# Kernel optimization log

Hardware: AMD Instinct MI355X
Metric: run time of the kernel (lower is better)

The kernel has to match this reference:

```python
import math
import jax, jax.numpy as jnp
import numpy as np

H = 16  # head_count

def setup_inputs() -> dict:
    key = jax.random.key(0)
    ks = jax.random.split(key, 7)
    B, S, D = 2, 2048, 1024
    query = jax.random.normal(ks[0], (B, S, D), dtype=jnp.float32)
    # mask: True = masked position (matches masked_fill_ semantics)
    mask = jax.random.randint(ks[1], (B, S, S), 0, 2) > 0
    scale = 1.0 / math.sqrt(D)  # xavier-ish init scale
    Wq = jax.random.normal(ks[2], (D, D), dtype=jnp.float32) * scale
    Wk = jax.random.normal(ks[3], (D, D), dtype=jnp.float32) * scale
    Wv = jax.random.normal(ks[4], (D, D), dtype=jnp.float32) * scale
    Wo = jax.random.normal(ks[5], (D, D), dtype=jnp.float32) * scale
    bo = jnp.zeros((D,), dtype=jnp.float32)
    return {"query": query, "mask": mask, "Wq": Wq, "Wk": Wk, "Wv": Wv, "Wo": Wo, "bo": bo}


def reference(query, mask, Wq, Wk, Wv, Wo, bo):
    B, S, D = query.shape
    dh = D // H

    def split_heads(x):  # [B,S,D] -> [B,H,S,dh]
        return x.reshape(B, S, H, dh).transpose(0, 2, 1, 3)

    # torch nn.Linear computes x @ W.T (bias-free for q/k/v)
    q = split_heads(query @ Wq.T) * (1.0 / math.sqrt(dh))
    k = split_heads(query @ Wk.T)
    v = split_heads(query @ Wv.T)

    scores = jnp.einsum('bhqd,bhkd->bhqk', q, k)           # [B,H,S,S]
    scores = jnp.where(mask[:, None, :, :], jnp.float32(-1e18), scores)
    weights = jax.nn.softmax(scores, axis=-1)               # dropout=0 -> identity
    ctx = jnp.einsum('bhqk,bhkd->bhqd', weights, v)         # [B,H,S,dh]
    ctx = ctx.transpose(0, 2, 1, 3).reshape(B, S, D)        # combine heads
    return ctx @ Wo.T + bo
```

## Files before the change

kernel.cpp:

```cpp
#include <hip/hip_runtime.h>

#define S_LEN 2048
#define D_MODEL 1024
#define NH 16
#define DH 64

typedef __bf16 bf16x8 __attribute__((ext_vector_type(8)));
typedef __bf16 bf16x4 __attribute__((ext_vector_type(4)));
typedef float f32x4 __attribute__((ext_vector_type(4)));

__device__ __forceinline__ unsigned short f2bf(float f) {
  unsigned int x = __float_as_uint(f);
  x += 0x7fffu + ((x >> 16) & 1u);
  return (unsigned short)(x >> 16);
}

__device__ __forceinline__ bf16x4 cvt4(f32x4 v) {
  return __builtin_convertvector(v, bf16x4);
}

__device__ __forceinline__ float exp2raw(float x) {
#if __has_builtin(__builtin_amdgcn_exp2f)
  return __builtin_amdgcn_exp2f(x);
#else
  return exp2f(x);
#endif
}

__device__ __forceinline__ f32x4 mfma16(bf16x8 a, bf16x8 b, f32x4 c) {
  return __builtin_amdgcn_mfma_f32_16x16x32_bf16(a, b, c, 0, 0, 0);
}

__device__ __forceinline__ void gl2lds(const unsigned short* g, unsigned short* l) {
  __builtin_amdgcn_global_load_lds(
      (__attribute__((address_space(1))) void*)g,
      (__attribute__((address_space(3))) void*)l, 16, 0, 0);
}

__global__ __launch_bounds__(256) void prep_kernel(
    const float* __restrict__ q, const float* __restrict__ wq,
    const float* __restrict__ wk, const float* __restrict__ wv,
    const float* __restrict__ wo, const int* __restrict__ mask,
    unsigned short* __restrict__ qbf, unsigned short* __restrict__ wbf,
    unsigned long long* __restrict__ bits) {
  const int bx = blockIdx.x;
  if (bx < 32768) {
    int i = bx * 256 + threadIdx.x;
    unsigned long long bal = __ballot(mask[i] != 0);
    if ((threadIdx.x & 63) == 0) bits[i >> 6] = bal;
  } else {
    const long t = (long)(bx - 32768) * 256 + threadIdx.x;
    const float* src;
    unsigned short* dst;
    long e;
    if (t < 524288) { src = q; dst = qbf; e = t * 8; }
    else {
      long u = t - 524288;
      int wi = (int)(u >> 17);
      e = (u & 131071) * 8;
      src = wi == 0 ? wq : wi == 1 ? wk : wi == 2 ? wv : wo;
      dst = wbf + (long)wi * 1048576;
    }
    float4 a = *(const float4*)(src + e);
    float4 b = *(const float4*)(src + e + 4);
    ushort4 p0 = {f2bf(a.x), f2bf(a.y), f2bf(a.z), f2bf(a.w)};
    ushort4 p1 = {f2bf(b.x), f2bf(b.y), f2bf(b.z), f2bf(b.w)};
    *(ushort4*)(dst + e) = p0;
    *(ushort4*)(dst + e + 4) = p1;
  }
}

__global__ __launch_bounds__(256) void gemm_qkv(
    const unsigned short* __restrict__ A, const unsigned short* __restrict__ W3,
    unsigned short* __restrict__ qb, unsigned short* __restrict__ kb,
    unsigned short* __restrict__ vt, float qscale) {
  __shared__ unsigned short As[128 * 64];
  __shared__ unsigned short Bs[128 * 64];
  const int tid = threadIdx.x, lane = tid & 63, wid = tid >> 6;
  const int wm = wid >> 1, wn = wid & 1;
  const int quad = lane >> 4, c = lane & 15, cx = c & 7;
  const int nG = blockIdx.x * 128;
  const int wi = nG >> 10, nn0 = nG & 1023;
  const int m0 = blockIdx.y * 128;
  const unsigned short* Bsrc = W3 + (size_t)wi * 1048576;
  const int srow = lane >> 3;
  const int schk = ((lane & 7) ^ srow) * 8;
  const unsigned short* ag = A + (size_t)(m0 + wid * 32 + srow) * 1024 + schk;
  const unsigned short* bg = Bsrc + (size_t)(nn0 + wid * 32 + srow) * 1024 + schk;
  f32x4 acc[4][4] = {};
  if (wi < 2) {
    for (int kk = 0; kk < 1024; kk += 64) {
#pragma unroll
      for (int i = 0; i < 4; ++i) {
        gl2lds(ag + (size_t)(i * 8) * 1024 + kk, &As[(wid * 32 + i * 8) * 64]);
        gl2lds(bg + (size_t)(i * 8) * 1024 + kk, &Bs[(wid * 32 + i * 8) * 64]);
      }
      __syncthreads();
#pragma unroll
      for (int kc = 0; kc < 2; ++kc) {
        bf16x8 a[4], b[4];
#pragma unroll
        for (int mt = 0; mt < 4; ++mt)
          a[mt] = *(const bf16x8*)(
              &As[(wm * 64 + mt * 16 + c) * 64 + ((kc * 4 + quad) ^ cx) * 8]);
#pragma unroll
        for (int nt = 0; nt < 4; ++nt)
          b[nt] = *(const bf16x8*)(
              &Bs[(wn * 64 + nt * 16 + c) * 64 + ((kc * 4 + quad) ^ cx) * 8]);
#pragma unroll
        for (int mt = 0; mt < 4; ++mt)
#pragma unroll
          for (int nt = 0; nt < 4; ++nt)
            acc[mt][nt] = mfma16(b[nt], a[mt], acc[mt][nt]);
      }
      __syncthreads();
    }
    unsigned short* dst = (wi == 0) ? qb : kb;
    const float sc = (wi == 0) ? qscale : 1.0f;
#pragma unroll
    for (int mt = 0; mt < 4; ++mt) {
#pragma unroll
      for (int nt = 0; nt < 4; ++nt) {
        const int ss = m0 + wm * 64 + mt * 16 + c;
        const int nS = nn0 + wn * 64 + nt * 16 + quad * 4;
        const int hh = nS >> 6, d0 = nS & 63;
        const int bb = ss >> 11, sl = ss & 2047;
        f32x4 v = acc[mt][nt] * sc;
        *(bf16x4*)(dst + (size_t)((bb * NH + hh) * S_LEN + sl) * DH + d0) =
            cvt4(v);
      }
    }
  } else {
    for (int kk = 0; kk < 1024; kk += 64) {
#pragma unroll
      for (int i = 0; i < 4; ++i) {
        gl2lds(ag + (size_t)(i * 8) * 1024 + kk, &As[(wid * 32 + i * 8) * 64]);
        gl2lds(bg + (size_t)(i * 8) * 1024 + kk, &Bs[(wid * 32 + i * 8) * 64]);
      }
      __syncthreads();
#pragma unroll
      for (int kc = 0; kc < 2; ++kc) {
        bf16x8 a[4], b[4];
#pragma unroll
        for (int mt = 0; mt < 4; ++mt)
          a[mt] = *(const bf16x8*)(
              &As[(wm * 64 + mt * 16 + c) * 64 + ((kc * 4 + quad) ^ cx) * 8]);
#pragma unroll
        for (int nt = 0; nt < 4; ++nt)
          b[nt] = *(const bf16x8*)(
              &Bs[(wn * 64 + nt * 16 + c) * 64 + ((kc * 4 + quad) ^ cx) * 8]);
#pragma unroll
        for (int mt = 0; mt < 4; ++mt)
#pragma unroll
          for (int nt = 0; nt < 4; ++nt)
            acc[mt][nt] = mfma16(a[mt], b[nt], acc[mt][nt]);
      }
      __syncthreads();
    }
#pragma unroll
    for (int mt = 0; mt < 4; ++mt) {
#pragma unroll
      for (int nt = 0; nt < 4; ++nt) {
        const int mb = m0 + wm * 64 + mt * 16 + quad * 4;
        const int n = nn0 + wn * 64 + nt * 16 + c;
        const int hh = n >> 6, d = n & 63;
        const int bb = mb >> 11, ss = mb & 2047;
        *(bf16x4*)(vt + (size_t)((bb * NH + hh) * DH + d) * S_LEN + ss) =
            cvt4(acc[mt][nt]);
      }
    }
  }
}

__global__ __launch_bounds__(256) void gemm_out(
    const unsigned short* __restrict__ A, const unsigned short* __restrict__ W,
    float* __restrict__ out, const float* __restrict__ bias) {
  __shared__ unsigned short As[128 * 64];
  __shared__ unsigned short Bs[64 * 64];
  const int tid = threadIdx.x, lane = tid & 63, wid = tid >> 6;
  const int wm = wid >> 1, wn = wid & 1;
  const int quad = lane >> 4, c = lane & 15, cx = c & 7;
  const int n0 = blockIdx.x * 64, m0 = blockIdx.y * 128;
  const int srow = lane >> 3;
  const int schk = ((lane & 7) ^ srow) * 8;
  const unsigned short* ag = A + (size_t)(m0 + wid * 32 + srow) * 1024 + schk;
  const unsigned short* bg = W + (size_t)(n0 + wid * 16 + srow) * 1024 + schk;
  f32x4 acc[4][2] = {};
  for (int kk = 0; kk < 1024; kk += 64) {
#pragma unroll
    for (int i = 0; i < 4; ++i)
      gl2lds(ag + (size_t)(i * 8) * 1024 + kk, &As[(wid * 32 + i * 8) * 64]);
#pragma unroll
    for (int i = 0; i < 2; ++i)
      gl2lds(bg + (size_t)(i * 8) * 1024 + kk, &Bs[(wid * 16 + i * 8) * 64]);
    __syncthreads();
#pragma unroll
    for (int kc = 0; kc < 2; ++kc) {
      bf16x8 a[4], b[2];
#pragma unroll
      for (int mt = 0; mt < 4; ++mt)
        a[mt] = *(const bf16x8*)(
            &As[(wm * 64 + mt * 16 + c) * 64 + ((kc * 4 + quad) ^ cx) * 8]);
#pragma unroll
      for (int nt = 0; nt < 2; ++nt)
        b[nt] = *(const bf16x8*)(
            &Bs[(wn * 32 + nt * 16 + c) * 64 + ((kc * 4 + quad) ^ cx) * 8]);
#pragma unroll
      for (int mt = 0; mt < 4; ++mt)
#pragma unroll
        for (int nt = 0; nt < 2; ++nt)
          acc[mt][nt] = mfma16(b[nt], a[mt], acc[mt][nt]);
    }
    __syncthreads();
  }
#pragma unroll
  for (int mt = 0; mt < 4; ++mt) {
#pragma unroll
    for (int nt = 0; nt < 2; ++nt) {
      const int m = m0 + wm * 64 + mt * 16 + c;
      const int n = n0 + wn * 32 + nt * 16 + quad * 4;
      f32x4 bv = *(const f32x4*)(bias + n);
      f32x4 r = acc[mt][nt] + bv;
      *(f32x4*)(out + (size_t)m * D_MODEL + n) = r;
    }
  }
}

__global__ __launch_bounds__(256, 2) void attn_kernel(
    const unsigned short* __restrict__ qb, const unsigned short* __restrict__ kb,
    const unsigned short* __restrict__ vt,
    const unsigned long long* __restrict__ mbits,
    unsigned short* __restrict__ ctx) {
  const int h = blockIdx.x, qt = blockIdx.y, b = blockIdx.z;
  const int bh = b * NH + h;
  const int tid = threadIdx.x, lane = tid & 63, wid = tid >> 6;
  const int quad = lane >> 4, c = lane & 15, cx = c & 7;
  const int qw = wid & 1, kh = wid >> 1;
  const int q0 = qt * 128;
  __shared__ __align__(16) unsigned short KVw[4][8192];
  __shared__ __align__(16) unsigned short Pbuf[4][16 * 72];

  const int qbase = q0 + qw * 64;
  const unsigned short* qp = qb + (size_t)(bh * S_LEN + qbase + c) * DH;
  bf16x8 bq[4][2];
#pragma unroll
  for (int sub = 0; sub < 4; ++sub) {
    bq[sub][0] = *(const bf16x8*)(qp + sub * 16 * DH + quad * 8);
    bq[sub][1] = *(const bf16x8*)(qp + sub * 16 * DH + 32 + quad * 8);
  }

  f32x4 o[4][4] = {};
  float lacc[4] = {0.f, 0.f, 0.f, 0.f};
  const unsigned long long* mq0 =
      mbits + (size_t)(b * S_LEN + qbase + c) * 32 + kh * 16;

  const int srow = lane >> 3;
  const int schk = ((lane & 7) ^ srow) * 8;
  unsigned short* Kw = KVw[wid];
  unsigned short* Vw = KVw[wid] + 4096;
  unsigned short* Pw = Pbuf[wid];

  const unsigned short* gK =
      kb + (size_t)(bh * S_LEN + kh * 1024 + srow) * DH + schk;
  const unsigned short* gV =
      vt + (size_t)(bh * DH + srow) * S_LEN + kh * 1024 + schk;

#pragma unroll
  for (int i = 0; i < 8; ++i) gl2lds(gK + (size_t)(i * 8) * DH, &Kw[i * 512]);
#pragma unroll
  for (int i = 0; i < 8; ++i)
    gl2lds(gV + (size_t)(i * 8) * S_LEN, &Vw[i * 512]);

  for (int kt = 0; kt < 1024; kt += 64) {
    asm volatile("s_waitcnt vmcnt(8)" ::: "memory");

    bf16x8 kf[8];
#pragma unroll
    for (int g = 0; g < 4; ++g) {
      const int rho = g * 16 + c;
      kf[2 * g] = *(const bf16x8*)(&Kw[rho * 64 + (quad ^ cx) * 8]);
      kf[2 * g + 1] = *(const bf16x8*)(&Kw[rho * 64 + ((4 + quad) ^ cx) * 8]);
    }

    const int mi = kt >> 6;
    bf16x8 bp[4][2];
#pragma unroll
    for (int sub = 0; sub < 4; ++sub) {
      f32x4 s[4];
#pragma unroll
      for (int g = 0; g < 4; ++g) {
        f32x4 z = {};
        z = mfma16(kf[2 * g], bq[sub][0], z);
        z = mfma16(kf[2 * g + 1], bq[sub][1], z);
        s[g] = z;
      }
      const unsigned long long w64 = mq0[sub * 512 + mi];
      const unsigned int wlo = (unsigned int)w64;
      const unsigned int whi = (unsigned int)(w64 >> 32);
      float lp = 0.f;
#pragma unroll
      for (int g = 0; g < 4; ++g) {
        const unsigned int bits =
            ((g & 2) ? whi : wlo) >> ((g & 1) * 16 + quad * 4);
        f32x4 p;
#pragma unroll
        for (int r = 0; r < 4; ++r) {
          const float e = exp2raw(s[g][r]);
          p[r] = ((bits >> r) & 1u) ? 0.f : e;
          lp += p[r];
        }
        *(bf16x4*)(&Pw[c * 72 + g * 16 + quad * 4]) = cvt4(p);
      }
      lacc[sub] += lp;
      bp[sub][0] = *(const bf16x8*)(&Pw[c * 72 + quad * 8]);
      bp[sub][1] = *(const bf16x8*)(&Pw[c * 72 + 32 + quad * 8]);
    }

    if (kt + 64 < 1024) {
#pragma unroll
      for (int i = 0; i < 8; ++i)
        gl2lds(gK + (size_t)(kt + 64 + i * 8) * DH, &Kw[i * 512]);
      asm volatile("s_waitcnt vmcnt(8)" ::: "memory");
    } else {
      asm volatile("s_waitcnt vmcnt(0)" ::: "memory");
    }

#pragma unroll
    for (int ks = 0; ks < 2; ++ks) {
#pragma unroll
      for (int nt = 0; nt < 4; ++nt) {
        bf16x8 av = *(const bf16x8*)(
            &Vw[(nt * 16 + c) * 64 + ((ks * 4 + quad) ^ cx) * 8]);
#pragma unroll
        for (int sub = 0; sub < 4; ++sub)
          o[sub][nt] = mfma16(av, bp[sub][ks], o[sub][nt]);
      }
    }
    asm volatile("s_waitcnt lgkmcnt(0)" ::: "memory");
    if (kt + 64 < 1024) {
#pragma unroll
      for (int i = 0; i < 8; ++i)
        gl2lds(gV + (size_t)(i * 8) * S_LEN + kt + 64, &Vw[i * 512]);
    }
  }

#pragma unroll
  for (int sub = 0; sub < 4; ++sub) {
    lacc[sub] += __shfl_xor(lacc[sub], 16, 64);
    lacc[sub] += __shfl_xor(lacc[sub], 32, 64);
  }

  __syncthreads();
  float* mrg = (float*)&KVw[0][0];
  float* ml = mrg + 8 * 1088;
  if (kh == 1) {
#pragma unroll
    for (int sub = 0; sub < 4; ++sub) {
      float* mo = mrg + (qw * 4 + sub) * 1088;
#pragma unroll
      for (int nt = 0; nt < 4; ++nt)
        *(f32x4*)(mo + c * 68 + nt * 16 + quad * 4) = o[sub][nt];
      if (quad == 0) ml[(qw * 4 + sub) * 16 + c] = lacc[sub];
    }
  }
  __syncthreads();
  if (kh == 0) {
#pragma unroll
    for (int sub = 0; sub < 4; ++sub) {
      const int pp = qw * 4 + sub;
      const float inv = 1.0f / (lacc[sub] + ml[pp * 16 + c]);
      const int q = qbase + sub * 16 + c;
      const float* mo = mrg + pp * 1088;
#pragma unroll
      for (int nt = 0; nt < 4; ++nt) {
        f32x4 ob = *(const f32x4*)(mo + c * 68 + nt * 16 + quad * 4);
        f32x4 rr = (o[sub][nt] + ob) * inv;
        *(bf16x4*)(ctx + (size_t)(b * S_LEN + q) * D_MODEL + h * DH + nt * 16 +
                   quad * 4) = cvt4(rr);
      }
    }
  }
}

extern "C" void kernel_launch(void* const* d_in, const int* in_sizes, int n_in,
                              void* d_out, int out_size, void* d_ws, size_t ws_size,
                              hipStream_t stream) {
  const float* query = (const float*)d_in[0];
  const int* mask = (const int*)d_in[1];
  const float* Wq = (const float*)d_in[2];
  const float* Wk = (const float*)d_in[3];
  const float* Wv = (const float*)d_in[4];
  const float* Wo = (const float*)d_in[5];
  const float* bo = (const float*)d_in[6];
  float* out = (float*)d_out;

  char* ws = (char*)d_ws;
  const size_t MB = 1024 * 1024;
  unsigned short* qbf = (unsigned short*)(ws);
  unsigned short* wbf = (unsigned short*)(ws + 8 * MB);
  unsigned short* qb = (unsigned short*)(ws + 16 * MB);
  unsigned short* kb = (unsigned short*)(ws + 24 * MB);
  unsigned short* vt = (unsigned short*)(ws + 32 * MB);
  unsigned long long* mb = (unsigned long long*)(ws + 40 * MB);
  unsigned short* ctx = qbf;

  prep_kernel<<<32768 + 4096, 256, 0, stream>>>(query, Wq, Wk, Wv, Wo, mask,
                                                qbf, wbf, mb);

  gemm_qkv<<<dim3(3072 / 128, 4096 / 128), 256, 0, stream>>>(
      qbf, wbf, qb, kb, vt, 0.18033688f);

  attn_kernel<<<dim3(NH, S_LEN / 128, 2), 256, 0, stream>>>(qb, kb, vt, mb,
                                                            ctx);

  gemm_out<<<dim3(1024 / 64, 4096 / 128), 256, 0, stream>>>(
      ctx, wbf + 3 * 1048576, out, bo);
}
```

Before: 224.6 us.

## Double-buffer GEMM K-tiles and prefetch attention mask words and K tiles earlier

The QKV and output GEMMs move from single-buffered 64-wide K tiles with two barriers per step to double-buffered 32-wide tiles with one barrier per step. The next tile's global-to-LDS copy is issued before the current tile is computed. The XOR swizzle is dropped, which may add LDS bank conflicts. In attention, the mask words for the next key tile are loaded one iteration ahead and the next K tile copy is issued before the softmax work, to hide load latency. This adds register pressure and relies on the hand-written vmcnt waits still counting the right loads.

```diff
diff --git a/kernel.cpp b/kernel.cpp
--- a/kernel.cpp
+++ b/kernel.cpp
@@ -74,46 +74,45 @@
     const unsigned short* __restrict__ A, const unsigned short* __restrict__ W3,
     unsigned short* __restrict__ qb, unsigned short* __restrict__ kb,
     unsigned short* __restrict__ vt, float qscale) {
-  __shared__ unsigned short As[128 * 64];
-  __shared__ unsigned short Bs[128 * 64];
+  __shared__ unsigned short As[2][128 * 32];
+  __shared__ unsigned short Bs[2][128 * 32];
   const int tid = threadIdx.x, lane = tid & 63, wid = tid >> 6;
   const int wm = wid >> 1, wn = wid & 1;
-  const int quad = lane >> 4, c = lane & 15, cx = c & 7;
+  const int quad = lane >> 4, c = lane & 15;
   const int nG = blockIdx.x * 128;
   const int wi = nG >> 10, nn0 = nG & 1023;
   const int m0 = blockIdx.y * 128;
-  const unsigned short* Bsrc = W3 + (size_t)wi * 1048576;
-  const int srow = lane >> 3;
-  const int schk = ((lane & 7) ^ srow) * 8;
-  const unsigned short* ag = A + (size_t)(m0 + wid * 32 + srow) * 1024 + schk;
-  const unsigned short* bg = Bsrc + (size_t)(nn0 + wid * 32 + srow) * 1024 + schk;
+  const int srow = lane >> 2, sc4 = (lane & 3) * 8;
+  const unsigned short* ag = A + (size_t)(m0 + wid * 32 + srow) * 1024 + sc4;
+  const unsigned short* bg =
+      W3 + (size_t)wi * 1048576 + (size_t)(nn0 + wid * 32 + srow) * 1024 + sc4;
   f32x4 acc[4][4] = {};
+  gl2lds(ag, &As[0][(wid * 32) * 32]);
+  gl2lds(ag + 16 * 1024, &As[0][(wid * 32 + 16) * 32]);
+  gl2lds(bg, &Bs[0][(wid * 32) * 32]);
+  gl2lds(bg + 16 * 1024, &Bs[0][(wid * 32 + 16) * 32]);
   if (wi < 2) {
-    for (int kk = 0; kk < 1024; kk += 64) {
-#pragma unroll
-      for (int i = 0; i < 4; ++i) {
-        gl2lds(ag + (size_t)(i * 8) * 1024 + kk, &As[(wid * 32 + i * 8) * 64]);
-        gl2lds(bg + (size_t)(i * 8) * 1024 + kk, &Bs[(wid * 32 + i * 8) * 64]);
-      }
+    for (int kk = 0; kk < 1024; kk += 32) {
+      const int pb = (kk >> 5) & 1;
       __syncthreads();
-#pragma unroll
-      for (int kc = 0; kc < 2; ++kc) {
-        bf16x8 a[4], b[4];
-#pragma unroll
-        for (int mt = 0; mt < 4; ++mt)
-          a[mt] = *(const bf16x8*)(
-              &As[(wm * 64 + mt * 16 + c) * 64 + ((kc * 4 + quad) ^ cx) * 8]);
+      if (kk + 32 < 1024) {
+        gl2lds(ag + kk + 32, &As[pb ^ 1][(wid * 32) * 32]);
+        gl2lds(ag + 16 * 1024 + kk + 32, &As[pb ^ 1][(wid * 32 + 16) * 32]);
+        gl2lds(bg + kk + 32, &Bs[pb ^ 1][(wid * 32) * 32]);
+        gl2lds(bg + 16 * 1024 + kk + 32, &Bs[pb ^ 1][(wid * 32 + 16) * 32]);
+      }
+      bf16x8 a[4], b[4];
+#pragma unroll
+      for (int mt = 0; mt < 4; ++mt)
+        a[mt] = *(const bf16x8*)(&As[pb][(wm * 64 + mt * 16 + c) * 32 + quad * 8]);
+#pragma unroll
+      for (int nt = 0; nt < 4; ++nt)
+        b[nt] = *(const bf16x8*)(&Bs[pb][(wn * 64 + nt * 16 + c) * 32 + quad * 8]);
+#pragma unroll
+      for (int mt = 0; mt < 4; ++mt)
 #pragma unroll
         for (int nt = 0; nt < 4; ++nt)
-          b[nt] = *(const bf16x8*)(
-              &Bs[(wn * 64 + nt * 16 + c) * 64 + ((kc * 4 + quad) ^ cx) * 8]);
-#pragma unroll
-        for (int mt = 0; mt < 4; ++mt)
-#pragma unroll
-          for (int nt = 0; nt < 4; ++nt)
-            acc[mt][nt] = mfma16(b[nt], a[mt], acc[mt][nt]);
-      }
-      __syncthreads();
+          acc[mt][nt] = mfma16(b[nt], a[mt], acc[mt][nt]);
     }
     unsigned short* dst = (wi == 0) ? qb : kb;
     const float sc = (wi == 0) ? qscale : 1.0f;
@@ -131,31 +130,27 @@
       }
     }
   } else {
-    for (int kk = 0; kk < 1024; kk += 64) {
-#pragma unroll
-      for (int i = 0; i < 4; ++i) {
-        gl2lds(ag + (size_t)(i * 8) * 1024 + kk, &As[(wid * 32 + i * 8) * 64]);
-        gl2lds(bg + (size_t)(i * 8) * 1024 + kk, &Bs[(wid * 32 + i * 8) * 64]);
-      }
+    for (int kk = 0; kk < 1024; kk += 32) {
+      const int pb = (kk >> 5) & 1;
       __syncthreads();
-#pragma unroll
-      for (int kc = 0; kc < 2; ++kc) {
-        bf16x8 a[4], b[4];
-#pragma unroll
-        for (int mt = 0; mt < 4; ++mt)
-          a[mt] = *(const bf16x8*)(
-              &As[(wm * 64 + mt * 16 + c) * 64 + ((kc * 4 + quad) ^ cx) * 8]);
+      if (kk + 32 < 1024) {
+        gl2lds(ag + kk + 32, &As[pb ^ 1][(wid * 32) * 32]);
+        gl2lds(ag + 16 * 1024 + kk + 32, &As[pb ^ 1][(wid * 32 + 16) * 32]);
+        gl2lds(bg + kk + 32, &Bs[pb ^ 1][(wid * 32) * 32]);
+        gl2lds(bg + 16 * 1024 + kk + 32, &Bs[pb ^ 1][(wid * 32 + 16) * 32]);
+      }
+      bf16x8 a[4], b[4];
+#pragma unroll
+      for (int mt = 0; mt < 4; ++mt)
+        a[mt] = *(const bf16x8*)(&As[pb][(wm * 64 + mt * 16 + c) * 32 + quad * 8]);
+#pragma unroll
+      for (int nt = 0; nt < 4; ++nt)
+        b[nt] = *(const bf16x8*)(&Bs[pb][(wn * 64 + nt * 16 + c) * 32 + quad * 8]);
+#pragma unroll
+      for (int mt = 0; mt < 4; ++mt)
 #pragma unroll
         for (int nt = 0; nt < 4; ++nt)
-          b[nt] = *(const bf16x8*)(
-              &Bs[(wn * 64 + nt * 16 + c) * 64 + ((kc * 4 + quad) ^ cx) * 8]);
-#pragma unroll
-        for (int mt = 0; mt < 4; ++mt)
-#pragma unroll
-          for (int nt = 0; nt < 4; ++nt)
-            acc[mt][nt] = mfma16(a[mt], b[nt], acc[mt][nt]);
-      }
-      __syncthreads();
+          acc[mt][nt] = mfma16(a[mt], b[nt], acc[mt][nt]);
     }
 #pragma unroll
     for (int mt = 0; mt < 4; ++mt) {
@@ -175,43 +170,39 @@
 __global__ __launch_bounds__(256) void gemm_out(
     const unsigned short* __restrict__ A, const unsigned short* __restrict__ W,
     float* __restrict__ out, const float* __restrict__ bias) {
-  __shared__ unsigned short As[128 * 64];
-  __shared__ unsigned short Bs[64 * 64];
+  __shared__ unsigned short As[2][128 * 32];
+  __shared__ unsigned short Bs[2][64 * 32];
   const int tid = threadIdx.x, lane = tid & 63, wid = tid >> 6;
   const int wm = wid >> 1, wn = wid & 1;
-  const int quad = lane >> 4, c = lane & 15, cx = c & 7;
+  const int quad = lane >> 4, c = lane & 15;
   const int n0 = blockIdx.x * 64, m0 = blockIdx.y * 128;
-  const int srow = lane >> 3;
-  const int schk = ((lane & 7) ^ srow) * 8;
-  const unsigned short* ag = A + (size_t)(m0 + wid * 32 + srow) * 1024 + schk;
-  const unsigned short* bg = W + (size_t)(n0 + wid * 16 + srow) * 1024 + schk;
+  const int srow = lane >> 2, sc4 = (lane & 3) * 8;
+  const unsigned short* ag = A + (size_t)(m0 + wid * 32 + srow) * 1024 + sc4;
+  const unsigned short* bg = W + (size_t)(n0 + wid * 16 + srow) * 1024 + sc4;
   f32x4 acc[4][2] = {};
-  for (int kk = 0; kk < 1024; kk += 64) {
-#pragma unroll
-    for (int i = 0; i < 4; ++i)
-      gl2lds(ag + (size_t)(i * 8) * 1024 + kk, &As[(wid * 32 + i * 8) * 64]);
-#pragma unroll
-    for (int i = 0; i < 2; ++i)
-      gl2lds(bg + (size_t)(i * 8) * 1024 + kk, &Bs[(wid * 16 + i * 8) * 64]);
+  gl2lds(ag, &As[0][(wid * 32) * 32]);
+  gl2lds(ag + 16 * 1024, &As[0][(wid * 32 + 16) * 32]);
+  gl2lds(bg, &Bs[0][(wid * 16) * 32]);
+  for (int kk = 0; kk < 1024; kk += 32) {
+    const int pb = (kk >> 5) & 1;
     __syncthreads();
-#pragma unroll
-    for (int kc = 0; kc < 2; ++kc) {
-      bf16x8 a[4], b[2];
-#pragma unroll
-      for (int mt = 0; mt < 4; ++mt)
-        a[mt] = *(const bf16x8*)(
-            &As[(wm * 64 + mt * 16 + c) * 64 + ((kc * 4 + quad) ^ cx) * 8]);
+    if (kk + 32 < 1024) {
+      gl2lds(ag + kk + 32, &As[pb ^ 1][(wid * 32) * 32]);
+      gl2lds(ag + 16 * 1024 + kk + 32, &As[pb ^ 1][(wid * 32 + 16) * 32]);
+      gl2lds(bg + kk + 32, &Bs[pb ^ 1][(wid * 16) * 32]);
+    }
+    bf16x8 a[4], b[2];
+#pragma unroll
+    for (int mt = 0; mt < 4; ++mt)
+      a[mt] = *(const bf16x8*)(&As[pb][(wm * 64 + mt * 16 + c) * 32 + quad * 8]);
+#pragma unroll
+    for (int nt = 0; nt < 2; ++nt)
+      b[nt] = *(const bf16x8*)(&Bs[pb][(wn * 32 + nt * 16 + c) * 32 + quad * 8]);
+#pragma unroll
+    for (int mt = 0; mt < 4; ++mt)
 #pragma unroll
       for (int nt = 0; nt < 2; ++nt)
-        b[nt] = *(const bf16x8*)(
-            &Bs[(wn * 32 + nt * 16 + c) * 64 + ((kc * 4 + quad) ^ cx) * 8]);
-#pragma unroll
-      for (int mt = 0; mt < 4; ++mt)
-#pragma unroll
-        for (int nt = 0; nt < 2; ++nt)
-          acc[mt][nt] = mfma16(b[nt], a[mt], acc[mt][nt]);
-    }
-    __syncthreads();
+        acc[mt][nt] = mfma16(b[nt], a[mt], acc[mt][nt]);
   }
 #pragma unroll
   for (int mt = 0; mt < 4; ++mt) {
@@ -254,6 +245,10 @@
   const unsigned long long* mq0 =
       mbits + (size_t)(b * S_LEN + qbase + c) * 32 + kh * 16;
 
+  unsigned long long mw[4];
+#pragma unroll
+  for (int sub = 0; sub < 4; ++sub) mw[sub] = mq0[sub * 512];
+
   const int srow = lane >> 3;
   const int schk = ((lane & 7) ^ srow) * 8;
   unsigned short* Kw = KVw[wid];
@@ -281,8 +276,18 @@
       kf[2 * g] = *(const bf16x8*)(&Kw[rho * 64 + (quad ^ cx) * 8]);
       kf[2 * g + 1] = *(const bf16x8*)(&Kw[rho * 64 + ((4 + quad) ^ cx) * 8]);
     }
-
-    const int mi = kt >> 6;
+    asm volatile("s_waitcnt lgkmcnt(0)" ::: "memory");
+
+    unsigned long long mwn[4];
+    if (kt + 64 < 1024) {
+      const int min = (kt >> 6) + 1;
+#pragma unroll
+      for (int sub = 0; sub < 4; ++sub) mwn[sub] = mq0[sub * 512 + min];
+#pragma unroll
+      for (int i = 0; i < 8; ++i)
+        gl2lds(gK + (size_t)(kt + 64 + i * 8) * DH, &Kw[i * 512]);
+    }
+
     bf16x8 bp[4][2];
 #pragma unroll
     for (int sub = 0; sub < 4; ++sub) {
@@ -294,9 +299,8 @@
         z = mfma16(kf[2 * g + 1], bq[sub][1], z);
         s[g] = z;
       }
-      const unsigned long long w64 = mq0[sub * 512 + mi];
-      const unsigned int wlo = (unsigned int)w64;
-      const unsigned int whi = (unsigned int)(w64 >> 32);
+      const unsigned int wlo = (unsigned int)mw[sub];
+      const unsigned int whi = (unsigned int)(mw[sub] >> 32);
       float lp = 0.f;
 #pragma unroll
       for (int g = 0; g < 4; ++g) {
@@ -317,10 +321,9 @@
     }
 
     if (kt + 64 < 1024) {
-#pragma unroll
-      for (int i = 0; i < 8; ++i)
-        gl2lds(gK + (size_t)(kt + 64 + i * 8) * DH, &Kw[i * 512]);
       asm volatile("s_waitcnt vmcnt(8)" ::: "memory");
+#pragma unroll
+      for (int sub = 0; sub < 4; ++sub) mw[sub] = mwn[sub];
     } else {
       asm volatile("s_waitcnt vmcnt(0)" ::: "memory");
     }
```

Measured after the change: 230.2 us. +2.5%, slower.

## Fuse fp32-to-bf16 conversion and mask packing into GEMM kernels, prefetch mask words

Applied to the files above, without the earlier changes.

Removes the separate prep kernel: the QKV and output GEMMs now read fp32 activations and weights directly and convert them to bf16 while staging into LDS, and mask bit-packing runs as extra blocks of the QKV GEMM launch. The attention kernel preloads the mask words for the next key tile and issues the next K tile load earlier, overlapping it with the softmax work. This saves a launch and the round trip through bf16 workspace copies. In exchange each GEMM block reads twice the bytes per tile, uses synchronous register-staged loads instead of direct global-to-LDS loads, and converts the same tiles redundantly across blocks.

```diff
diff --git a/kernel.cpp b/kernel.cpp
--- a/kernel.cpp
+++ b/kernel.cpp
@@ -37,63 +37,56 @@
       (__attribute__((address_space(3))) void*)l, 16, 0, 0);
 }
 
-__global__ __launch_bounds__(256) void prep_kernel(
-    const float* __restrict__ q, const float* __restrict__ wq,
-    const float* __restrict__ wk, const float* __restrict__ wv,
-    const float* __restrict__ wo, const int* __restrict__ mask,
-    unsigned short* __restrict__ qbf, unsigned short* __restrict__ wbf,
-    unsigned long long* __restrict__ bits) {
+__device__ __forceinline__ void cvt_stage(unsigned short* dst,
+                                          const float* __restrict__ src) {
+  float4 a0 = *(const float4*)(src);
+  float4 a1 = *(const float4*)(src + 4);
+  ushort4 p0 = {f2bf(a0.x), f2bf(a0.y), f2bf(a0.z), f2bf(a0.w)};
+  ushort4 p1 = {f2bf(a1.x), f2bf(a1.y), f2bf(a1.z), f2bf(a1.w)};
+  *(ushort4*)(dst) = p0;
+  *(ushort4*)(dst + 4) = p1;
+}
+
+__global__ __launch_bounds__(256) void gemm_qkv(
+    const float* __restrict__ Q, const float* __restrict__ Wq,
+    const float* __restrict__ Wk, const float* __restrict__ Wv,
+    const int* __restrict__ mask, unsigned short* __restrict__ qb,
+    unsigned short* __restrict__ kb, unsigned short* __restrict__ vt,
+    unsigned long long* __restrict__ bits, float qscale) {
   const int bx = blockIdx.x;
-  if (bx < 32768) {
-    int i = bx * 256 + threadIdx.x;
-    unsigned long long bal = __ballot(mask[i] != 0);
-    if ((threadIdx.x & 63) == 0) bits[i >> 6] = bal;
-  } else {
-    const long t = (long)(bx - 32768) * 256 + threadIdx.x;
-    const float* src;
-    unsigned short* dst;
-    long e;
-    if (t < 524288) { src = q; dst = qbf; e = t * 8; }
-    else {
-      long u = t - 524288;
-      int wi = (int)(u >> 17);
-      e = (u & 131071) * 8;
-      src = wi == 0 ? wq : wi == 1 ? wk : wi == 2 ? wv : wo;
-      dst = wbf + (long)wi * 1048576;
-    }
-    float4 a = *(const float4*)(src + e);
-    float4 b = *(const float4*)(src + e + 4);
-    ushort4 p0 = {f2bf(a.x), f2bf(a.y), f2bf(a.z), f2bf(a.w)};
-    ushort4 p1 = {f2bf(b.x), f2bf(b.y), f2bf(b.z), f2bf(b.w)};
-    *(ushort4*)(dst + e) = p0;
-    *(ushort4*)(dst + e + 4) = p1;
-  }
-}
-
-__global__ __launch_bounds__(256) void gemm_qkv(
-    const unsigned short* __restrict__ A, const unsigned short* __restrict__ W3,
-    unsigned short* __restrict__ qb, unsigned short* __restrict__ kb,
-    unsigned short* __restrict__ vt, float qscale) {
+  if (bx >= 768) {
+    const int base = (bx - 768) * 1024 + threadIdx.x;
+#pragma unroll
+    for (int r = 0; r < 4; ++r) {
+      const int i = base + r * 256;
+      unsigned long long bal = __ballot(mask[i] != 0);
+      if ((threadIdx.x & 63) == 0) bits[i >> 6] = bal;
+    }
+    return;
+  }
   __shared__ unsigned short As[128 * 64];
   __shared__ unsigned short Bs[128 * 64];
   const int tid = threadIdx.x, lane = tid & 63, wid = tid >> 6;
   const int wm = wid >> 1, wn = wid & 1;
   const int quad = lane >> 4, c = lane & 15, cx = c & 7;
-  const int nG = blockIdx.x * 128;
+  const int nG = (bx % 24) * 128;
   const int wi = nG >> 10, nn0 = nG & 1023;
-  const int m0 = blockIdx.y * 128;
-  const unsigned short* Bsrc = W3 + (size_t)wi * 1048576;
+  const int m0 = (bx / 24) * 128;
+  const float* Wsrc = (wi == 0) ? Wq : (wi == 1) ? Wk : Wv;
   const int srow = lane >> 3;
   const int schk = ((lane & 7) ^ srow) * 8;
-  const unsigned short* ag = A + (size_t)(m0 + wid * 32 + srow) * 1024 + schk;
-  const unsigned short* bg = Bsrc + (size_t)(nn0 + wid * 32 + srow) * 1024 + schk;
+  const float* ag = Q + (size_t)(m0 + wid * 32 + srow) * 1024 + schk;
+  const float* bg = Wsrc + (size_t)(nn0 + wid * 32 + srow) * 1024 + schk;
+  const int dchk = (lane & 7) * 8;
   f32x4 acc[4][4] = {};
   if (wi < 2) {
     for (int kk = 0; kk < 1024; kk += 64) {
 #pragma unroll
       for (int i = 0; i < 4; ++i) {
-        gl2lds(ag + (size_t)(i * 8) * 1024 + kk, &As[(wid * 32 + i * 8) * 64]);
-        gl2lds(bg + (size_t)(i * 8) * 1024 + kk, &Bs[(wid * 32 + i * 8) * 64]);
+        cvt_stage(&As[(wid * 32 + i * 8 + srow) * 64 + dchk],
+                  ag + (size_t)(i * 8) * 1024 + kk);
+        cvt_stage(&Bs[(wid * 32 + i * 8 + srow) * 64 + dchk],
+                  bg + (size_t)(i * 8) * 1024 + kk);
       }
       __syncthreads();
 #pragma unroll
@@ -134,8 +127,10 @@
     for (int kk = 0; kk < 1024; kk += 64) {
 #pragma unroll
       for (int i = 0; i < 4; ++i) {
-        gl2lds(ag + (size_t)(i * 8) * 1024 + kk, &As[(wid * 32 + i * 8) * 64]);
-        gl2lds(bg + (size_t)(i * 8) * 1024 + kk, &Bs[(wid * 32 + i * 8) * 64]);
+        cvt_stage(&As[(wid * 32 + i * 8 + srow) * 64 + dchk],
+                  ag + (size_t)(i * 8) * 1024 + kk);
+        cvt_stage(&Bs[(wid * 32 + i * 8 + srow) * 64 + dchk],
+                  bg + (size_t)(i * 8) * 1024 + kk);
       }
       __syncthreads();
 #pragma unroll
@@ -173,7 +168,7 @@
 }
 
 __global__ __launch_bounds__(256) void gemm_out(
-    const unsigned short* __restrict__ A, const unsigned short* __restrict__ W,
+    const unsigned short* __restrict__ A, const float* __restrict__ W,
     float* __restrict__ out, const float* __restrict__ bias) {
   __shared__ unsigned short As[128 * 64];
   __shared__ unsigned short Bs[64 * 64];
@@ -183,8 +178,9 @@
   const int n0 = blockIdx.x * 64, m0 = blockIdx.y * 128;
   const int srow = lane >> 3;
   const int schk = ((lane & 7) ^ srow) * 8;
+  const int dchk = (lane & 7) * 8;
   const unsigned short* ag = A + (size_t)(m0 + wid * 32 + srow) * 1024 + schk;
-  const unsigned short* bg = W + (size_t)(n0 + wid * 16 + srow) * 1024 + schk;
+  const float* bg = W + (size_t)(n0 + wid * 16 + srow) * 1024 + schk;
   f32x4 acc[4][2] = {};
   for (int kk = 0; kk < 1024; kk += 64) {
 #pragma unroll
@@ -192,7 +188,8 @@
       gl2lds(ag + (size_t)(i * 8) * 1024 + kk, &As[(wid * 32 + i * 8) * 64]);
 #pragma unroll
     for (int i = 0; i < 2; ++i)
-      gl2lds(bg + (size_t)(i * 8) * 1024 + kk, &Bs[(wid * 16 + i * 8) * 64]);
+      cvt_stage(&Bs[(wid * 16 + i * 8 + srow) * 64 + dchk],
+                bg + (size_t)(i * 8) * 1024 + kk);
     __syncthreads();
 #pragma unroll
     for (int kc = 0; kc < 2; ++kc) {
@@ -254,6 +251,10 @@
   const unsigned long long* mq0 =
       mbits + (size_t)(b * S_LEN + qbase + c) * 32 + kh * 16;
 
+  unsigned long long mw[4];
+#pragma unroll
+  for (int sub = 0; sub < 4; ++sub) mw[sub] = mq0[sub * 512];
+
   const int srow = lane >> 3;
   const int schk = ((lane & 7) ^ srow) * 8;
   unsigned short* Kw = KVw[wid];
@@ -281,8 +282,18 @@
       kf[2 * g] = *(const bf16x8*)(&Kw[rho * 64 + (quad ^ cx) * 8]);
       kf[2 * g + 1] = *(const bf16x8*)(&Kw[rho * 64 + ((4 + quad) ^ cx) * 8]);
     }
-
-    const int mi = kt >> 6;
+    asm volatile("s_waitcnt lgkmcnt(0)" ::: "memory");
+
+    unsigned long long mwn[4];
+    if (kt + 64 < 1024) {
+      const int min = (kt >> 6) + 1;
+#pragma unroll
+      for (int sub = 0; sub < 4; ++sub) mwn[sub] = mq0[sub * 512 + min];
+#pragma unroll
+      for (int i = 0; i < 8; ++i)
+        gl2lds(gK + (size_t)(kt + 64 + i * 8) * DH, &Kw[i * 512]);
+    }
+
     bf16x8 bp[4][2];
 #pragma unroll
     for (int sub = 0; sub < 4; ++sub) {
@@ -294,9 +305,8 @@
         z = mfma16(kf[2 * g + 1], bq[sub][1], z);
         s[g] = z;
       }
-      const unsigned long long w64 = mq0[sub * 512 + mi];
-      const unsigned int wlo = (unsigned int)w64;
-      const unsigned int whi = (unsigned int)(w64 >> 32);
+      const unsigned int wlo = (unsigned int)mw[sub];
+      const unsigned int whi = (unsigned int)(mw[sub] >> 32);
       float lp = 0.f;
 #pragma unroll
       for (int g = 0; g < 4; ++g) {
@@ -317,10 +327,9 @@
     }
 
     if (kt + 64 < 1024) {
-#pragma unroll
-      for (int i = 0; i < 8; ++i)
-        gl2lds(gK + (size_t)(kt + 64 + i * 8) * DH, &Kw[i * 512]);
       asm volatile("s_waitcnt vmcnt(8)" ::: "memory");
+#pragma unroll
+      for (int sub = 0; sub < 4; ++sub) mw[sub] = mwn[sub];
     } else {
       asm volatile("s_waitcnt vmcnt(0)" ::: "memory");
     }
@@ -396,23 +405,17 @@
 
   char* ws = (char*)d_ws;
   const size_t MB = 1024 * 1024;
-  unsigned short* qbf = (unsigned short*)(ws);
-  unsigned short* wbf = (unsigned short*)(ws + 8 * MB);
-  unsigned short* qb = (unsigned short*)(ws + 16 * MB);
-  unsigned short* kb = (unsigned short*)(ws + 24 * MB);
-  unsigned short* vt = (unsigned short*)(ws + 32 * MB);
-  unsigned long long* mb = (unsigned long long*)(ws + 40 * MB);
-  unsigned short* ctx = qbf;
-
-  prep_kernel<<<32768 + 4096, 256, 0, stream>>>(query, Wq, Wk, Wv, Wo, mask,
-                                                qbf, wbf, mb);
-
-  gemm_qkv<<<dim3(3072 / 128, 4096 / 128), 256, 0, stream>>>(
-      qbf, wbf, qb, kb, vt, 0.18033688f);
+  unsigned short* ctx = (unsigned short*)(ws);
+  unsigned short* qb = (unsigned short*)(ws + 8 * MB);
+  unsigned short* kb = (unsigned short*)(ws + 16 * MB);
+  unsigned short* vt = (unsigned short*)(ws + 24 * MB);
+  unsigned long long* mb = (unsigned long long*)(ws + 32 * MB);
+
+  gemm_qkv<<<768 + 8192, 256, 0, stream>>>(query, Wq, Wk, Wv, mask, qb, kb, vt,
+                                           mb, 0.18033688f);
 
   attn_kernel<<<dim3(NH, S_LEN / 128, 2), 256, 0, stream>>>(qb, kb, vt, mb,
                                                             ctx);
 
-  gemm_out<<<dim3(1024 / 64, 4096 / 128), 256, 0, stream>>>(
-      ctx, wbf + 3 * 1048576, out, bo);
-}
+  gemm_out<<<dim3(1024 / 64, 4096 / 128), 256, 0, stream>>>(ctx, Wo, out, bo);
+}
```

Result: slower. 267.8 us (+19.2%).
